# Optimization experiments

Measured on AMD Instinct MI355X. Metric: run time of the kernel, lower is better.

The kernel has to match this reference:

```python
import jax, jax.numpy as jnp
import numpy as np
import math

D_MODEL = 512
N_HEADS = 8
D_K = D_MODEL // N_HEADS
D_FF = 2048
EPS = 1e-6


def _layer_norm(x, gamma, beta):
    # Matches the torch module: unbiased std (ddof=1), divide by (std + eps)
    mean = jnp.mean(x, axis=-1, keepdims=True)
    std = jnp.std(x, axis=-1, ddof=1, keepdims=True)
    return gamma * (x - mean) / (std + EPS) + beta


def setup_inputs() -> dict:
    key = jax.random.key(0)
    ks = jax.random.split(key, 16)
    B, S = 4, 2048
    s_attn = 1.0 / math.sqrt(D_MODEL)
    s_ff1 = 1.0 / math.sqrt(D_MODEL)
    s_ff2 = 1.0 / math.sqrt(D_FF)
    inp = {
        "x": jax.random.normal(ks[0], (B, S, D_MODEL), dtype=jnp.float32),
        "mask": jnp.ones((1, 1, S, S), dtype=jnp.int32),
        "wq": jax.random.normal(ks[1], (D_MODEL, D_MODEL), jnp.float32) * s_attn,
        "bq": jnp.zeros((D_MODEL,), jnp.float32),
        "wk": jax.random.normal(ks[2], (D_MODEL, D_MODEL), jnp.float32) * s_attn,
        "bk": jnp.zeros((D_MODEL,), jnp.float32),
        "wv": jax.random.normal(ks[3], (D_MODEL, D_MODEL), jnp.float32) * s_attn,
        "bv": jnp.zeros((D_MODEL,), jnp.float32),
        "wo": jax.random.normal(ks[4], (D_MODEL, D_MODEL), jnp.float32) * s_attn,
        "bo": jnp.zeros((D_MODEL,), jnp.float32),
        "w1": jax.random.normal(ks[5], (D_MODEL, D_FF), jnp.float32) * s_ff1,
        "b1": jnp.zeros((D_FF,), jnp.float32),
        "w2": jax.random.normal(ks[6], (D_FF, D_MODEL), jnp.float32) * s_ff2,
        "b2": jnp.zeros((D_MODEL,), jnp.float32),
        "g1": jnp.ones((1, 1, D_MODEL), jnp.float32),
        "be1": jnp.zeros((1, 1, D_MODEL), jnp.float32),
        "g2": jnp.ones((1, 1, D_MODEL), jnp.float32),
        "be2": jnp.zeros((1, 1, D_MODEL), jnp.float32),
    }
    return inp


def reference(x, mask, wq, bq, wk, bk, wv, bv, wo, bo, w1, b1, w2, b2, g1, be1, g2, be2):
    B, S, _ = x.shape
    # --- residual 1: pre-norm self-attention ---
    xn = _layer_norm(x, g1, be1)
    q = (xn @ wq + bq).reshape(B, S, N_HEADS, D_K).transpose(0, 2, 1, 3)
    k = (xn @ wk + bk).reshape(B, S, N_HEADS, D_K).transpose(0, 2, 1, 3)
    v = (xn @ wv + bv).reshape(B, S, N_HEADS, D_K).transpose(0, 2, 1, 3)
    # NOTE: source uses floor division `//` by sqrt(d_k) (a faithful-ly kept bug)
    scores = jnp.floor_divide(jnp.einsum("bhqd,bhkd->bhqk", q, k), math.sqrt(D_K))
    scores = jnp.where(mask == 0, jnp.float32(-1e9), scores)
    attn = jax.nn.softmax(scores, axis=-1)
    ctx = jnp.einsum("bhqk,bhkd->bhqd", attn, v)
    ctx = ctx.transpose(0, 2, 1, 3).reshape(B, S, D_MODEL)
    x = x + (ctx @ wo + bo)
    # --- residual 2: pre-norm feed-forward ---
    xn2 = _layer_norm(x, g2, be2)
    ff = jax.nn.relu(xn2 @ w1 + b1) @ w2 + b2
    return x + ff
```

## Files before the change

kernel.cpp:

```cpp
#include <hip/hip_runtime.h>
#include <cmath>

#define SEQ 2048
#define DM 512
#define DFF 2048
#define NH 8
#define DKH 64
#define NROWS 8192

typedef __attribute__((ext_vector_type(8))) short bf16x8;
typedef __attribute__((ext_vector_type(16))) float f32x16;

__device__ __forceinline__ ushort f2bf(float f) {
    uint u = __float_as_uint(f);
    u += 0x7fff + ((u >> 16) & 1);
    return (ushort)(u >> 16);
}
__device__ __forceinline__ float bf2f(ushort h) {
    return __uint_as_float(((uint)h) << 16);
}
__device__ __forceinline__ uint cvtpk_bf16(float a, float b) {
    uint r;
    asm("v_cvt_pk_bf16_f32 %0, %1, %2" : "=v"(r) : "v"(a), "v"(b));
    return r;
}
__device__ __forceinline__ void gl_lds16(const void* g, void* l) {
    __builtin_amdgcn_global_load_lds(
        (const __attribute__((address_space(1))) void*)g,
        (__attribute__((address_space(3))) void*)l, 16, 0, 0);
}
__device__ __forceinline__ void* swz(char* base, int row, int col) {
    int byte = (row << 7) + (col << 1);
    byte ^= (row & 7) << 4;
    return base + byte;
}
__device__ __forceinline__ void* swzg(char* base, int row, int k) {
    int byte = (row << 7) + (k << 1);
    byte ^= ((row >> 2) & 7) << 4;
    return base + byte;
}

template<bool SPLIT>
__global__ __launch_bounds__(64) void ln_kernel(const float* __restrict__ x,
        const float* __restrict__ g, const float* __restrict__ b,
        ushort* __restrict__ oh, ushort* __restrict__ ol) {
    int row = blockIdx.x;
    int t = threadIdx.x;
    const float* xr = x + (size_t)row * DM + t * 8;
    float v[8];
    *(float4*)&v[0] = *(const float4*)(xr);
    *(float4*)&v[4] = *(const float4*)(xr + 4);
    float s = 0.f;
    #pragma unroll
    for (int j = 0; j < 8; ++j) s += v[j];
    #pragma unroll
    for (int m = 32; m > 0; m >>= 1) s += __shfl_xor(s, m);
    float mean = s * (1.0f / DM);
    float ss = 0.f;
    #pragma unroll
    for (int j = 0; j < 8; ++j) { float d = v[j] - mean; ss += d * d; }
    #pragma unroll
    for (int m = 32; m > 0; m >>= 1) ss += __shfl_xor(ss, m);
    float inv = 1.0f / (sqrtf(ss * (1.0f / (DM - 1))) + 1e-6f);
    float gv[8], bv[8];
    *(float4*)&gv[0] = *(const float4*)(g + t * 8);
    *(float4*)&gv[4] = *(const float4*)(g + t * 8 + 4);
    *(float4*)&bv[0] = *(const float4*)(b + t * 8);
    *(float4*)&bv[4] = *(const float4*)(b + t * 8 + 4);
    union { ushort us[8]; float4 f4; } ph, pl;
    #pragma unroll
    for (int j = 0; j < 8; ++j) {
        float o = gv[j] * (v[j] - mean) * inv + bv[j];
        ushort hb = f2bf(o);
        ph.us[j] = hb;
        if (SPLIT) pl.us[j] = f2bf(o - bf2f(hb));
    }
    *(float4*)(oh + (size_t)row * DM + t * 8) = ph.f4;
    if (SPLIT) *(float4*)(ol + (size_t)row * DM + t * 8) = pl.f4;
}

__global__ __launch_bounds__(256) void wconv4(
        const float* __restrict__ wq, const float* __restrict__ wk,
        const float* __restrict__ wv, const float* __restrict__ wo,
        ushort* __restrict__ qh, ushort* __restrict__ ql,
        ushort* __restrict__ kh, ushort* __restrict__ kl,
        ushort* __restrict__ vh, ushort* __restrict__ oh) {
    const int K = DM, N = DM;
    __shared__ float tile[64][65];
    int z = blockIdx.z;
    const float* W = (z == 0) ? wq : (z == 1) ? wk : (z == 2) ? wv : wo;
    ushort* Th = (z == 0) ? qh : (z == 1) ? kh : (z == 2) ? vh : oh;
    ushort* Tl = (z == 0) ? ql : (z == 1) ? kl : nullptr;
    bool split = (z < 2);
    int k0 = blockIdx.x * 64, n0 = blockIdx.y * 64;
    int t = threadIdx.x;
    {
        int kr = t >> 2, c0 = (t & 3) * 16;
        const float* src = W + (size_t)(k0 + kr) * N + n0 + c0;
        #pragma unroll
        for (int j = 0; j < 4; ++j)
            *(float4*)&tile[kr][c0 + j * 4] = *(const float4*)(src + j * 4);
    }
    __syncthreads();
    int n = t >> 2, kc = (t & 3) * 16;
    union { ushort us[16]; float4 f4[2]; } ph, pl;
    #pragma unroll
    for (int j = 0; j < 16; ++j) {
        float v = tile[kc + j][n];
        ushort hb = f2bf(v);
        ph.us[j] = hb;
        pl.us[j] = f2bf(v - bf2f(hb));
    }
    ushort* dh = Th + (size_t)(n0 + n) * K + k0 + kc;
    *(float4*)(dh) = ph.f4[0];
    *(float4*)(dh + 8) = ph.f4[1];
    if (split) {
        ushort* dl = Tl + (size_t)(n0 + n) * K + k0 + kc;
        *(float4*)(dl) = pl.f4[0];
        *(float4*)(dl + 8) = pl.f4[1];
    }
}

__global__ __launch_bounds__(256) void wconv(const float* __restrict__ W,
        ushort* __restrict__ Th, int K, int N) {
    __shared__ float tile[64][65];
    int k0 = blockIdx.x * 64, n0 = blockIdx.y * 64;
    int t = threadIdx.x;
    {
        int kr = t >> 2, c0 = (t & 3) * 16;
        const float* src = W + (size_t)(k0 + kr) * N + n0 + c0;
        #pragma unroll
        for (int j = 0; j < 4; ++j)
            *(float4*)&tile[kr][c0 + j * 4] = *(const float4*)(src + j * 4);
    }
    __syncthreads();
    int n = t >> 2, kc = (t & 3) * 16;
    union { ushort us[16]; float4 f4[2]; } ph;
    #pragma unroll
    for (int j = 0; j < 16; ++j) ph.us[j] = f2bf(tile[kc + j][n]);
    ushort* dh = Th + (size_t)(n0 + n) * K + k0 + kc;
    *(float4*)(dh) = ph.f4[0];
    *(float4*)(dh + 8) = ph.f4[1];
}

__global__ __launch_bounds__(256) void vtrans(const ushort* __restrict__ vh,
        ushort* __restrict__ vt) {
    __shared__ __align__(16) char tile[8192];
    int s0 = blockIdx.x * 64;
    int bh = blockIdx.y;
    int b = bh >> 3, h = bh & 7;
    int t = threadIdx.x;
    {
        int r = t >> 2, co = (t & 3) * 16;
        const ushort* src = vh + (size_t)(b * SEQ + s0 + r) * DM + h * DKH + co;
        *(float4*)swz(tile, r, co) = *(const float4*)(src);
        *(float4*)swz(tile, r, co + 8) = *(const float4*)(src + 8);
    }
    __syncthreads();
    int d = t >> 2, j0 = (t & 3) * 16;
    union { ushort us[16]; float4 f4[2]; } o;
    #pragma unroll
    for (int j = 0; j < 16; ++j)
        o.us[j] = *(ushort*)swz(tile, j0 + j, d);
    ushort* dst = vt + ((size_t)bh * DKH + d) * SEQ + s0 + j0;
    *(float4*)(dst) = o.f4[0];
    *(float4*)(dst + 8) = o.f4[1];
}

__global__ __launch_bounds__(256) void maskprep(const int* __restrict__ mask,
        ushort* __restrict__ mb) {
    int i = (blockIdx.x * 256 + threadIdx.x) * 8;
    int4 a = *(const int4*)(mask + i);
    int4 c = *(const int4*)(mask + i + 4);
    ushort neg = f2bf(-1e9f);
    union { ushort us[8]; float4 f4; } o;
    o.us[0] = a.x ? (ushort)0 : neg;
    o.us[1] = a.y ? (ushort)0 : neg;
    o.us[2] = a.z ? (ushort)0 : neg;
    o.us[3] = a.w ? (ushort)0 : neg;
    o.us[4] = c.x ? (ushort)0 : neg;
    o.us[5] = c.y ? (ushort)0 : neg;
    o.us[6] = c.z ? (ushort)0 : neg;
    o.us[7] = c.w ? (ushort)0 : neg;
    *(float4*)(mb + i) = o.f4;
}

template<bool RELU, bool HASRES, int OUT>
__global__ __launch_bounds__(256) void mgemm(
        const ushort* __restrict__ Ah, const ushort* __restrict__ Bth,
        const float* __restrict__ bias, const float* __restrict__ resid,
        float* __restrict__ Cf, ushort* __restrict__ Cbh,
        int M, int N, int K) {
    __shared__ __align__(16) char smem[65536];
    int tid = threadIdx.x;
    int lane = tid & 63, w = tid >> 6;
    int ln31 = lane & 31, hi = lane >> 5;
    int mh = (w >> 1) * 64, nh = (w & 1) * 64;
    int gx = gridDim.x;
    int nwg = gx * gridDim.y;
    int flat = blockIdx.y * gx + blockIdx.x;
    int sid = (flat & 7) * (nwg >> 3) + (flat >> 3);
    int n0 = (sid % gx) * 128;
    int m0 = (sid / gx) * 128;

    f32x16 acc[2][2];
    #pragma unroll
    for (int i = 0; i < 2; ++i)
        #pragma unroll
        for (int j = 0; j < 2; ++j)
            #pragma unroll
            for (int r = 0; r < 16; ++r) acc[i][j][r] = 0.f;

    auto stage = [&](char* Abuf, char* Bbuf, int k0) {
        #pragma unroll
        for (int c = 0; c < 4; ++c) {
            int ch = w * 4 + c;
            int r = ch * 8 + (lane >> 3);
            int u = (lane & 7) ^ ((r >> 2) & 7);
            gl_lds16(Ah + (size_t)(m0 + r) * K + k0 + u * 8, Abuf + ch * 1024);
            gl_lds16(Bth + (size_t)(n0 + r) * K + k0 + u * 8, Bbuf + ch * 1024);
        }
    };

    char* A0 = smem;
    char* B0 = smem + 16384;
    char* A1 = smem + 32768;
    char* B1 = smem + 49152;

    stage(A0, B0, 0);
    __syncthreads();
    int nk = K / 64;
    for (int kt = 0; kt < nk; ++kt) {
        char* Ac = (kt & 1) ? A1 : A0;
        char* Bc = (kt & 1) ? B1 : B0;
        if (kt + 1 < nk)
            stage((kt & 1) ? A0 : A1, (kt & 1) ? B0 : B1, (kt + 1) * 64);
        __builtin_amdgcn_s_setprio(1);
        #pragma unroll
        for (int km = 0; km < 4; ++km) {
            int kk = km * 16 + hi * 8;
            bf16x8 ah[2], bh[2];
            ah[0] = *(bf16x8*)swzg(Ac, mh + ln31, kk);
            ah[1] = *(bf16x8*)swzg(Ac, mh + 32 + ln31, kk);
            bh[0] = *(bf16x8*)swzg(Bc, nh + ln31, kk);
            bh[1] = *(bf16x8*)swzg(Bc, nh + 32 + ln31, kk);
            #pragma unroll
            for (int mi = 0; mi < 2; ++mi)
                #pragma unroll
                for (int ni = 0; ni < 2; ++ni)
                    acc[mi][ni] = __builtin_amdgcn_mfma_f32_32x32x16_bf16(
                        ah[mi], bh[ni], acc[mi][ni], 0, 0, 0);
        }
        __builtin_amdgcn_s_setprio(0);
        __syncthreads();
    }
    float bv[2];
    bv[0] = bias[n0 + nh + ln31];
    bv[1] = bias[n0 + nh + 32 + ln31];
    #pragma unroll
    for (int mi = 0; mi < 2; ++mi)
        #pragma unroll
        for (int ni = 0; ni < 2; ++ni) {
            int n = n0 + nh + ni * 32 + ln31;
            #pragma unroll
            for (int r = 0; r < 16; ++r) {
                int m = m0 + mh + mi * 32 + (r & 3) + 8 * (r >> 2) + 4 * hi;
                float v = acc[mi][ni][r] + bv[ni];
                if (HASRES) v += resid[(size_t)m * N + n];
                if (RELU) v = fmaxf(v, 0.f);
                size_t idx = (size_t)m * N + n;
                if (OUT == 0) Cf[idx] = v;
                else Cbh[idx] = f2bf(v);
            }
        }
}

__global__ __launch_bounds__(256) void qkv_gemm(
        const ushort* __restrict__ Ah, const ushort* __restrict__ Al,
        const ushort* __restrict__ Bth, const ushort* __restrict__ Btl,
        const float* __restrict__ bq, const float* __restrict__ bk,
        const float* __restrict__ bv_, ushort* __restrict__ q_h,
        ushort* __restrict__ q_l, ushort* __restrict__ k_h,
        ushort* __restrict__ k_l, ushort* __restrict__ v_h) {
    const int K = DM, N = DM;
    __shared__ __align__(16) char smem[65536];
    char* As_h = smem;
    char* Bs_h = smem + 16384;
    char* As_l = smem + 32768;
    char* Bs_l = smem + 49152;
    int tid = threadIdx.x;
    int lane = tid & 63, w = tid >> 6;
    int ln31 = lane & 31, hi = lane >> 5;
    int mh = (w >> 1) * 64, nh = (w & 1) * 64;
    int gx = gridDim.x;
    int nwg = gx * gridDim.y;
    int flat = blockIdx.y * gx + blockIdx.x;
    int sid = (flat & 7) * (nwg >> 3) + (flat >> 3);
    int n0 = (sid % gx) * 128;
    int m0 = (sid / gx) * 128;
    bool isqk = (n0 < 1024);

    f32x16 acc[2][2];
    #pragma unroll
    for (int i = 0; i < 2; ++i)
        #pragma unroll
        for (int j = 0; j < 2; ++j)
            #pragma unroll
            for (int r = 0; r < 16; ++r) acc[i][j][r] = 0.f;

    for (int k0 = 0; k0 < K; k0 += 64) {
        #pragma unroll
        for (int c = 0; c < 4; ++c) {
            int ch = w * 4 + c;
            int r = ch * 8 + (lane >> 3);
            int u = (lane & 7) ^ ((r >> 2) & 7);
            gl_lds16(Ah + (size_t)(m0 + r) * K + k0 + u * 8, As_h + ch * 1024);
            gl_lds16(Bth + (size_t)(n0 + r) * K + k0 + u * 8, Bs_h + ch * 1024);
            if (isqk) {
                gl_lds16(Al + (size_t)(m0 + r) * K + k0 + u * 8, As_l + ch * 1024);
                gl_lds16(Btl + (size_t)(n0 + r) * K + k0 + u * 8, Bs_l + ch * 1024);
            }
        }
        __syncthreads();
        __builtin_amdgcn_s_setprio(1);
        #pragma unroll
        for (int km = 0; km < 4; ++km) {
            int kk = km * 16 + hi * 8;
            bf16x8 ah[2], bh[2];
            ah[0] = *(bf16x8*)swzg(As_h, mh + ln31, kk);
            ah[1] = *(bf16x8*)swzg(As_h, mh + 32 + ln31, kk);
            bh[0] = *(bf16x8*)swzg(Bs_h, nh + ln31, kk);
            bh[1] = *(bf16x8*)swzg(Bs_h, nh + 32 + ln31, kk);
            if (isqk) {
                bf16x8 al[2], bl[2];
                al[0] = *(bf16x8*)swzg(As_l, mh + ln31, kk);
                al[1] = *(bf16x8*)swzg(As_l, mh + 32 + ln31, kk);
                bl[0] = *(bf16x8*)swzg(Bs_l, nh + ln31, kk);
                bl[1] = *(bf16x8*)swzg(Bs_l, nh + 32 + ln31, kk);
                #pragma unroll
                for (int mi = 0; mi < 2; ++mi)
                    #pragma unroll
                    for (int ni = 0; ni < 2; ++ni) {
                        acc[mi][ni] = __builtin_amdgcn_mfma_f32_32x32x16_bf16(
                            ah[mi], bh[ni], acc[mi][ni], 0, 0, 0);
                        acc[mi][ni] = __builtin_amdgcn_mfma_f32_32x32x16_bf16(
                            ah[mi], bl[ni], acc[mi][ni], 0, 0, 0);
                        acc[mi][ni] = __builtin_amdgcn_mfma_f32_32x32x16_bf16(
                            al[mi], bh[ni], acc[mi][ni], 0, 0, 0);
                    }
            } else {
                #pragma unroll
                for (int mi = 0; mi < 2; ++mi)
                    #pragma unroll
                    for (int ni = 0; ni < 2; ++ni)
                        acc[mi][ni] = __builtin_amdgcn_mfma_f32_32x32x16_bf16(
                            ah[mi], bh[ni], acc[mi][ni], 0, 0, 0);
            }
        }
        __builtin_amdgcn_s_setprio(0);
        __syncthreads();
    }
    const float* bias = (n0 < 512) ? bq : (n0 < 1024 ? bk : bv_);
    int ncol0 = n0 & 511;
    ushort* Oh = (n0 < 512) ? q_h : (n0 < 1024 ? k_h : v_h);
    ushort* Ol = (n0 < 512) ? q_l : (n0 < 1024 ? k_l : nullptr);
    float bvv[2];
    bvv[0] = bias[ncol0 + nh + ln31];
    bvv[1] = bias[ncol0 + nh + 32 + ln31];
    #pragma unroll
    for (int mi = 0; mi < 2; ++mi)
        #pragma unroll
        for (int ni = 0; ni < 2; ++ni) {
            int n = ncol0 + nh + ni * 32 + ln31;
            #pragma unroll
            for (int r = 0; r < 16; ++r) {
                int m = m0 + mh + mi * 32 + (r & 3) + 8 * (r >> 2) + 4 * hi;
                float v = acc[mi][ni][r] + bvv[ni];
                size_t idx = (size_t)m * N + n;
                ushort hb = f2bf(v);
                Oh[idx] = hb;
                if (isqk) Ol[idx] = f2bf(v - bf2f(hb));
            }
        }
}

__global__ __launch_bounds__(256, 3) void attn_kernel(
        const ushort* __restrict__ Qh, const ushort* __restrict__ Ql,
        const ushort* __restrict__ Khg, const ushort* __restrict__ Klg,
        const ushort* __restrict__ Vtg, const ushort* __restrict__ mb,
        ushort* __restrict__ O) {
    __shared__ __align__(16) char smem[49152];
    int tid = threadIdx.x;
    int w = tid >> 6, lane = tid & 63;
    int ln31 = lane & 31, hi = lane >> 5;
    bool hib = (hi != 0);
    int f = blockIdx.y * gridDim.x + blockIdx.x;
    int g = (f & 7) * 64 + (f >> 3);
    int qb = g & 15, bh = g >> 4;
    int b = bh >> 3, h = bh & 7;
    int q0 = qb * 128;
    size_t brow = (size_t)b * SEQ;
    int hcol = h * DKH;

    auto stage_kv = [&](char* buf, int kt) {
        #pragma unroll
        for (int c = 0; c < 2; ++c) {
            int ch = w * 2 + c;
            int r = ch * 8 + (lane >> 3);
            int u = (lane & 7) ^ (r & 7);
            gl_lds16(Khg + (brow + kt * 64 + r) * DM + hcol + u * 8,
                     buf + ch * 1024);
            gl_lds16(Klg + (brow + kt * 64 + r) * DM + hcol + u * 8,
                     buf + 8192 + ch * 1024);
            gl_lds16(Vtg + ((size_t)bh * DKH + r) * SEQ + kt * 64 + u * 8,
                     buf + 16384 + ch * 1024);
        }
    };

    {
        char* QhL = smem;
        char* QlL = smem + 16384;
        #pragma unroll
        for (int c = 0; c < 4; ++c) {
            int ch = w * 4 + c;
            int r = ch * 8 + (lane >> 3);
            int u = (lane & 7) ^ (r & 7);
            gl_lds16(Qh + (brow + q0 + r) * DM + hcol + u * 8, QhL + ch * 1024);
            gl_lds16(Ql + (brow + q0 + r) * DM + hcol + u * 8, QlL + ch * 1024);
        }
    }
    __syncthreads();
    bf16x8 qfh[4], qfl[4];
    {
        int qr = w * 32 + ln31;
        #pragma unroll
        for (int c = 0; c < 4; ++c) {
            qfh[c] = *(bf16x8*)swz(smem, qr, c * 16 + hi * 8);
            qfl[c] = *(bf16x8*)swz(smem + 16384, qr, c * 16 + hi * 8);
        }
    }
    __syncthreads();
    stage_kv(smem, 0);
    __syncthreads();

    f32x16 ctx0, ctx1;
    #pragma unroll
    for (int r = 0; r < 16; ++r) { ctx0[r] = 0.f; ctx1[r] = 0.f; }
    float m_i = -1e30f, l_i = 0.f;
    int qglob = q0 + w * 32 + ln31;
    const ushort* mrow = mb + (size_t)qglob * SEQ;

    for (int kt = 0; kt < SEQ / 64; ++kt) {
        char* cur = smem + (kt & 1) * 24576;
        if (kt + 1 < SEQ / 64)
            stage_kv(smem + ((kt + 1) & 1) * 24576, kt + 1);
        ushort4 mpre[8];
        #pragma unroll
        for (int i = 0; i < 8; ++i)
            mpre[i] = *(const ushort4*)(mrow + kt * 64 + i * 8 + hi * 4);
        char* KhL = cur;
        char* KlL = cur + 8192;
        char* VtL = cur + 16384;
        #pragma unroll
        for (int ksub = 0; ksub < 2; ++ksub) {
            f32x16 s;
            #pragma unroll
            for (int r = 0; r < 16; ++r) s[r] = 0.f;
            __builtin_amdgcn_s_setprio(1);
            #pragma unroll
            for (int c = 0; c < 4; ++c) {
                bf16x8 ka = *(bf16x8*)swz(KhL, ksub * 32 + ln31, c * 16 + hi * 8);
                bf16x8 kb = *(bf16x8*)swz(KlL, ksub * 32 + ln31, c * 16 + hi * 8);
                s = __builtin_amdgcn_mfma_f32_32x32x16_bf16(ka, qfh[c], s, 0, 0, 0);
                s = __builtin_amdgcn_mfma_f32_32x32x16_bf16(ka, qfl[c], s, 0, 0, 0);
                s = __builtin_amdgcn_mfma_f32_32x32x16_bf16(kb, qfh[c], s, 0, 0, 0);
            }
            __builtin_amdgcn_s_setprio(0);
            float tmax = -1e30f;
            #pragma unroll
            for (int rg = 0; rg < 4; ++rg) {
                ushort4 mv = mpre[ksub * 4 + rg];
                ushort mu[4] = {mv.x, mv.y, mv.z, mv.w};
                #pragma unroll
                for (int j = 0; j < 4; ++j) {
                    int r = rg * 4 + j;
                    float sc = floorf(s[r] * 0.125f) + bf2f(mu[j]);
                    s[r] = sc;
                    tmax = fmaxf(tmax, sc);
                }
            }
            tmax = fmaxf(tmax, __shfl_xor(tmax, 32));
            if (!__all(tmax <= m_i)) {
                float newm = fmaxf(m_i, tmax);
                float scl = __expf(m_i - newm);
                m_i = newm;
                l_i *= scl;
                #pragma unroll
                for (int r = 0; r < 16; ++r) { ctx0[r] *= scl; ctx1[r] *= scl; }
            }
            float psum = 0.f;
            #pragma unroll
            for (int r = 0; r < 16; ++r) {
                float p = __expf(s[r] - m_i);
                s[r] = p;
                psum += p;
            }
            psum += __shfl_xor(psum, 32);
            l_i += psum;
            uint pk0[4], pk1[4];
            #pragma unroll
            for (int rg = 0; rg < 4; ++rg) {
                pk0[rg] = cvtpk_bf16(s[rg * 4 + 0], s[rg * 4 + 1]);
                pk1[rg] = cvtpk_bf16(s[rg * 4 + 2], s[rg * 4 + 3]);
            }
            __builtin_amdgcn_s_setprio(1);
            #pragma unroll
            for (int cc = 0; cc < 2; ++cc) {
                uint A0 = pk0[cc * 2], A1 = pk1[cc * 2];
                uint B0 = pk0[cc * 2 + 1], B1 = pk1[cc * 2 + 1];
                uint send0 = hib ? A0 : B0;
                uint send1 = hib ? A1 : B1;
                uint own0  = hib ? B0 : A0;
                uint own1  = hib ? B1 : A1;
                uint recv0 = (uint)__shfl_xor((int)send0, 32);
                uint recv1 = (uint)__shfl_xor((int)send1, 32);
                union { uint u[4]; bf16x8 v; } pb;
                pb.u[0] = hib ? recv0 : own0;
                pb.u[1] = hib ? recv1 : own1;
                pb.u[2] = hib ? own0 : recv0;
                pb.u[3] = hib ? own1 : recv1;
                int c = ksub * 2 + cc;
                bf16x8 va0 = *(bf16x8*)swz(VtL, ln31, c * 16 + hi * 8);
                bf16x8 va1 = *(bf16x8*)swz(VtL, 32 + ln31, c * 16 + hi * 8);
                ctx0 = __builtin_amdgcn_mfma_f32_32x32x16_bf16(va0, pb.v, ctx0, 0, 0, 0);
                ctx1 = __builtin_amdgcn_mfma_f32_32x32x16_bf16(va1, pb.v, ctx1, 0, 0, 0);
            }
            __builtin_amdgcn_s_setprio(0);
        }
        __syncthreads();
    }

    float inv = 1.0f / l_i;
    ushort* op = O + (brow + qglob) * DM + hcol;
    #pragma unroll
    for (int r = 0; r < 16; ++r) {
        int d = (r & 3) + 8 * (r >> 2) + 4 * hi;
        op[d] = f2bf(ctx0[r] * inv);
        op[32 + d] = f2bf(ctx1[r] * inv);
    }
}

extern "C" void kernel_launch(void* const* d_in, const int* in_sizes, int n_in,
                              void* d_out, int out_size, void* d_ws, size_t ws_size,
                              hipStream_t stream) {
    const float* x    = (const float*)d_in[0];
    const int*   mask = (const int*)d_in[1];
    const float* wq = (const float*)d_in[2];
    const float* bq = (const float*)d_in[3];
    const float* wk = (const float*)d_in[4];
    const float* bk = (const float*)d_in[5];
    const float* wv = (const float*)d_in[6];
    const float* bv = (const float*)d_in[7];
    const float* wo = (const float*)d_in[8];
    const float* bo = (const float*)d_in[9];
    const float* w1 = (const float*)d_in[10];
    const float* b1 = (const float*)d_in[11];
    const float* w2 = (const float*)d_in[12];
    const float* b2 = (const float*)d_in[13];
    const float* g1  = (const float*)d_in[14];
    const float* be1 = (const float*)d_in[15];
    const float* g2  = (const float*)d_in[16];
    const float* be2 = (const float*)d_in[17];
    float* out = (float*)d_out;

    char* ws = (char*)d_ws;
    const size_t MiB = 1024 * 1024;
    ushort* xn_h = (ushort*)(ws);
    ushort* xn_l = (ushort*)(ws + 8 * MiB);
    ushort* q_h  = (ushort*)(ws + 16 * MiB);
    ushort* q_l  = (ushort*)(ws + 24 * MiB);
    ushort* k_h  = (ushort*)(ws + 32 * MiB);
    ushort* k_l  = (ushort*)(ws + 40 * MiB);
    ushort* v_h  = (ushort*)(ws + 48 * MiB);
    ushort* v_t  = (ushort*)(ws + 56 * MiB);
    ushort* wqkvt_h = (ushort*)(ws + 64 * MiB);
    ushort* wqkvt_l = (ushort*)(ws + 66 * MiB);
    ushort* wot_h = (ushort*)(ws + 67 * MiB);
    ushort* w1t_h = (ushort*)(ws + 68 * MiB);
    ushort* w2t_h = (ushort*)(ws + 70 * MiB);
    ushort* mb    = (ushort*)(ws + 72 * MiB);
    ushort* ctx  = xn_h;
    ushort* xn2  = xn_l;
    ushort* ff1  = q_h;

    dim3 blk256(256);
    wconv4<<<dim3(8, 8, 4), blk256, 0, stream>>>(
        wq, wk, wv, wo, wqkvt_h, wqkvt_l, wqkvt_h + 512 * 512,
        wqkvt_l + 512 * 512, wqkvt_h + 1024 * 512, wot_h);
    wconv<<<dim3(8, 32), blk256, 0, stream>>>(w1, w1t_h, DM, DFF);
    wconv<<<dim3(32, 8), blk256, 0, stream>>>(w2, w2t_h, DFF, DM);
    maskprep<<<SEQ * SEQ / 8 / 256, blk256, 0, stream>>>(mask, mb);
    ln_kernel<true><<<NROWS, 64, 0, stream>>>(x, g1, be1, xn_h, xn_l);
    qkv_gemm<<<dim3(12, NROWS / 128), blk256, 0, stream>>>(
        xn_h, xn_l, wqkvt_h, wqkvt_l, bq, bk, bv, q_h, q_l, k_h, k_l, v_h);
    vtrans<<<dim3(SEQ / 64, 4 * NH), blk256, 0, stream>>>(v_h, v_t);
    {
        dim3 grid(SEQ / 128, 4 * NH);
        attn_kernel<<<grid, blk256, 0, stream>>>(q_h, q_l, k_h, k_l, v_t, mb, ctx);
    }
    {
        dim3 grid(DM / 128, NROWS / 128);
        mgemm<false,true,0><<<grid, blk256, 0, stream>>>(
            ctx, wot_h, bo, x, out, nullptr, NROWS, DM, DM);
    }
    ln_kernel<false><<<NROWS, 64, 0, stream>>>(out, g2, be2, xn2, nullptr);
    {
        dim3 grid(DFF / 128, NROWS / 128);
        mgemm<true,false,1><<<grid, blk256, 0, stream>>>(
            xn2, w1t_h, b1, nullptr, nullptr, ff1, NROWS, DFF, DM);
    }
    {
        dim3 grid(DM / 128, NROWS / 128);
        mgemm<false,true,0><<<grid, blk256, 0, stream>>>(
            ff1, w2t_h, b2, out, out, nullptr, NROWS, DM, DFF);
    }
}
```

Baseline: 240.7 us.

## Split attention over key halves with combine kernel and skip all-ones mask tiles

The attention kernel now splits the key range into two halves, doubling the grid to 1024 blocks. Each block writes unnormalized partial context plus its running max and sum, and a new combine kernel merges the two halves flash-decoding style. maskprep also builds per-row, per-64-key-tile flags marking tiles where the mask is all ones, so the attention loop skips the mask loads and adds there. This raises occupancy and cuts mask memory traffic, at the cost of an extra kernel, partial-result round trips through global memory, and bf16 rounding of the unnormalized partials.

```diff
diff --git a/kernel.cpp b/kernel.cpp
--- a/kernel.cpp
+++ b/kernel.cpp
@@ -167,22 +167,39 @@
     *(float4*)(dst + 8) = o.f4[1];
 }
 
-__global__ __launch_bounds__(256) void maskprep(const int* __restrict__ mask,
-        ushort* __restrict__ mb) {
-    int i = (blockIdx.x * 256 + threadIdx.x) * 8;
-    int4 a = *(const int4*)(mask + i);
-    int4 c = *(const int4*)(mask + i + 4);
+__global__ __launch_bounds__(64) void maskprep(const int* __restrict__ mask,
+        ushort* __restrict__ mb, unsigned char* __restrict__ mflag) {
+    int row = blockIdx.x;
+    int lane = threadIdx.x;
     ushort neg = f2bf(-1e9f);
-    union { ushort us[8]; float4 f4; } o;
-    o.us[0] = a.x ? (ushort)0 : neg;
-    o.us[1] = a.y ? (ushort)0 : neg;
-    o.us[2] = a.z ? (ushort)0 : neg;
-    o.us[3] = a.w ? (ushort)0 : neg;
-    o.us[4] = c.x ? (ushort)0 : neg;
-    o.us[5] = c.y ? (ushort)0 : neg;
-    o.us[6] = c.z ? (ushort)0 : neg;
-    o.us[7] = c.w ? (ushort)0 : neg;
-    *(float4*)(mb + i) = o.f4;
+    unsigned long long bal[4];
+    #pragma unroll
+    for (int u = 0; u < 4; ++u) {
+        int base = row * SEQ + u * 512 + lane * 8;
+        int4 a = *(const int4*)(mask + base);
+        int4 c = *(const int4*)(mask + base + 4);
+        union { ushort us[8]; float4 f4; } o;
+        o.us[0] = a.x ? (ushort)0 : neg;
+        o.us[1] = a.y ? (ushort)0 : neg;
+        o.us[2] = a.z ? (ushort)0 : neg;
+        o.us[3] = a.w ? (ushort)0 : neg;
+        o.us[4] = c.x ? (ushort)0 : neg;
+        o.us[5] = c.y ? (ushort)0 : neg;
+        o.us[6] = c.z ? (ushort)0 : neg;
+        o.us[7] = c.w ? (ushort)0 : neg;
+        *(float4*)(mb + base) = o.f4;
+        bool ok = a.x && a.y && a.z && a.w && c.x && c.y && c.z && c.w;
+        bal[u] = __ballot(ok);
+    }
+    if (lane < 32) {
+        int u = lane >> 3;
+        unsigned long long bsel = bal[0];
+        bsel = (u == 1) ? bal[1] : bsel;
+        bsel = (u == 2) ? bal[2] : bsel;
+        bsel = (u == 3) ? bal[3] : bsel;
+        int byte = (int)((bsel >> ((lane & 7) * 8)) & 0xFFull);
+        mflag[row * 32 + lane] = (byte == 0xFF) ? 1 : 0;
+    }
 }
 
 template<bool RELU, bool HASRES, int OUT>
@@ -388,19 +405,23 @@
         const ushort* __restrict__ Qh, const ushort* __restrict__ Ql,
         const ushort* __restrict__ Khg, const ushort* __restrict__ Klg,
         const ushort* __restrict__ Vtg, const ushort* __restrict__ mb,
-        ushort* __restrict__ O) {
+        const unsigned char* __restrict__ mflag,
+        ushort* __restrict__ pctx0, ushort* __restrict__ pctx1,
+        float2* __restrict__ ml) {
     __shared__ __align__(16) char smem[49152];
     int tid = threadIdx.x;
     int w = tid >> 6, lane = tid & 63;
     int ln31 = lane & 31, hi = lane >> 5;
     bool hib = (hi != 0);
     int f = blockIdx.y * gridDim.x + blockIdx.x;
-    int g = (f & 7) * 64 + (f >> 3);
-    int qb = g & 15, bh = g >> 4;
+    int g = (f & 7) * 128 + (f >> 3);
+    int bh = g >> 5, rest = g & 31;
+    int part = rest >> 4, qb = rest & 15;
     int b = bh >> 3, h = bh & 7;
     int q0 = qb * 128;
     size_t brow = (size_t)b * SEQ;
     int hcol = h * DKH;
+    int ktbeg = part * 16, ktend = ktbeg + 16;
 
     auto stage_kv = [&](char* buf, int kt) {
         #pragma unroll
@@ -440,7 +461,7 @@
         }
     }
     __syncthreads();
-    stage_kv(smem, 0);
+    stage_kv(smem + (ktbeg & 1) * 24576, ktbeg);
     __syncthreads();
 
     f32x16 ctx0, ctx1;
@@ -450,14 +471,18 @@
     int qglob = q0 + w * 32 + ln31;
     const ushort* mrow = mb + (size_t)qglob * SEQ;
 
-    for (int kt = 0; kt < SEQ / 64; ++kt) {
+    for (int kt = ktbeg; kt < ktend; ++kt) {
         char* cur = smem + (kt & 1) * 24576;
-        if (kt + 1 < SEQ / 64)
+        if (kt + 1 < ktend)
             stage_kv(smem + ((kt + 1) & 1) * 24576, kt + 1);
+        unsigned char fl = mflag[qglob * 32 + kt];
+        bool domask = !__all(fl != 0);
         ushort4 mpre[8];
-        #pragma unroll
-        for (int i = 0; i < 8; ++i)
-            mpre[i] = *(const ushort4*)(mrow + kt * 64 + i * 8 + hi * 4);
+        if (domask) {
+            #pragma unroll
+            for (int i = 0; i < 8; ++i)
+                mpre[i] = *(const ushort4*)(mrow + kt * 64 + i * 8 + hi * 4);
+        }
         char* KhL = cur;
         char* KlL = cur + 8192;
         char* VtL = cur + 16384;
@@ -477,14 +502,23 @@
             }
             __builtin_amdgcn_s_setprio(0);
             float tmax = -1e30f;
-            #pragma unroll
-            for (int rg = 0; rg < 4; ++rg) {
-                ushort4 mv = mpre[ksub * 4 + rg];
-                ushort mu[4] = {mv.x, mv.y, mv.z, mv.w};
+            if (domask) {
                 #pragma unroll
-                for (int j = 0; j < 4; ++j) {
-                    int r = rg * 4 + j;
-                    float sc = floorf(s[r] * 0.125f) + bf2f(mu[j]);
+                for (int rg = 0; rg < 4; ++rg) {
+                    ushort4 mv = mpre[ksub * 4 + rg];
+                    ushort mu[4] = {mv.x, mv.y, mv.z, mv.w};
+                    #pragma unroll
+                    for (int j = 0; j < 4; ++j) {
+                        int r = rg * 4 + j;
+                        float sc = floorf(s[r] * 0.125f) + bf2f(mu[j]);
+                        s[r] = sc;
+                        tmax = fmaxf(tmax, sc);
+                    }
+                }
+            } else {
+                #pragma unroll
+                for (int r = 0; r < 16; ++r) {
+                    float sc = floorf(s[r] * 0.125f);
                     s[r] = sc;
                     tmax = fmaxf(tmax, sc);
                 }
@@ -540,14 +574,42 @@
         __syncthreads();
     }
 
-    float inv = 1.0f / l_i;
-    ushort* op = O + (brow + qglob) * DM + hcol;
+    ushort* P = part ? pctx1 : pctx0;
+    size_t pbase = ((size_t)bh * SEQ + qglob) * DKH;
     #pragma unroll
     for (int r = 0; r < 16; ++r) {
         int d = (r & 3) + 8 * (r >> 2) + 4 * hi;
-        op[d] = f2bf(ctx0[r] * inv);
-        op[32 + d] = f2bf(ctx1[r] * inv);
-    }
+        P[pbase + d] = f2bf(ctx0[r]);
+        P[pbase + 32 + d] = f2bf(ctx1[r]);
+    }
+    if (hi == 0)
+        ml[((size_t)part * 32 + bh) * SEQ + qglob] = make_float2(m_i, l_i);
+}
+
+__global__ __launch_bounds__(256) void attn_combine(
+        const ushort* __restrict__ p0, const ushort* __restrict__ p1,
+        const float2* __restrict__ ml, ushort* __restrict__ O) {
+    int idx = blockIdx.x * 256 + threadIdx.x;
+    int d0 = (idx & 7) * 8;
+    int q = (idx >> 3) & (SEQ - 1);
+    int bh = idx >> 14;
+    int b = bh >> 3, h = bh & 7;
+    size_t pb = ((size_t)bh * SEQ + q) * DKH + d0;
+    bf16x8 c0 = *(const bf16x8*)(p0 + pb);
+    bf16x8 c1 = *(const bf16x8*)(p1 + pb);
+    float2 e0 = ml[(size_t)bh * SEQ + q];
+    float2 e1 = ml[((size_t)32 + bh) * SEQ + q];
+    float m = fmaxf(e0.x, e1.x);
+    float w0 = __expf(e0.x - m), w1 = __expf(e1.x - m);
+    float inv = 1.0f / (e0.y * w0 + e1.y * w1);
+    union { ushort us[8]; float4 f4; } o;
+    #pragma unroll
+    for (int j = 0; j < 8; ++j) {
+        float v0 = bf2f((ushort)c0[j]);
+        float v1 = bf2f((ushort)c1[j]);
+        o.us[j] = f2bf((v0 * w0 + v1 * w1) * inv);
+    }
+    *(float4*)(O + ((size_t)(b * SEQ + q)) * DM + h * DKH + d0) = o.f4;
 }
 
 extern "C" void kernel_launch(void* const* d_in, const int* in_sizes, int n_in,
@@ -586,9 +648,13 @@
     ushort* wqkvt_h = (ushort*)(ws + 64 * MiB);
     ushort* wqkvt_l = (ushort*)(ws + 66 * MiB);
     ushort* wot_h = (ushort*)(ws + 67 * MiB);
+    unsigned char* mflag = (unsigned char*)(ws + 67 * MiB + 512 * 1024);
     ushort* w1t_h = (ushort*)(ws + 68 * MiB);
     ushort* w2t_h = (ushort*)(ws + 70 * MiB);
     ushort* mb    = (ushort*)(ws + 72 * MiB);
+    ushort* pctx0 = (ushort*)(ws + 80 * MiB);
+    ushort* pctx1 = (ushort*)(ws + 88 * MiB);
+    float2* ml    = (float2*)(ws + 64 * MiB);
     ushort* ctx  = xn_h;
     ushort* xn2  = xn_l;
     ushort* ff1  = q_h;
@@ -599,15 +665,17 @@
         wqkvt_l + 512 * 512, wqkvt_h + 1024 * 512, wot_h);
     wconv<<<dim3(8, 32), blk256, 0, stream>>>(w1, w1t_h, DM, DFF);
     wconv<<<dim3(32, 8), blk256, 0, stream>>>(w2, w2t_h, DFF, DM);
-    maskprep<<<SEQ * SEQ / 8 / 256, blk256, 0, stream>>>(mask, mb);
+    maskprep<<<SEQ, 64, 0, stream>>>(mask, mb, mflag);
     ln_kernel<true><<<NROWS, 64, 0, stream>>>(x, g1, be1, xn_h, xn_l);
     qkv_gemm<<<dim3(12, NROWS / 128), blk256, 0, stream>>>(
         xn_h, xn_l, wqkvt_h, wqkvt_l, bq, bk, bv, q_h, q_l, k_h, k_l, v_h);
     vtrans<<<dim3(SEQ / 64, 4 * NH), blk256, 0, stream>>>(v_h, v_t);
     {
-        dim3 grid(SEQ / 128, 4 * NH);
-        attn_kernel<<<grid, blk256, 0, stream>>>(q_h, q_l, k_h, k_l, v_t, mb, ctx);
-    }
+        dim3 grid(32, 32);
+        attn_kernel<<<grid, blk256, 0, stream>>>(
+            q_h, q_l, k_h, k_l, v_t, mb, mflag, pctx0, pctx1, ml);
+    }
+    attn_combine<<<32 * SEQ * 8 / 256, blk256, 0, stream>>>(pctx0, pctx1, ml, ctx);
     {
         dim3 grid(DM / 128, NROWS / 128);
         mgemm<false,true,0><<<grid, blk256, 0, stream>>>(
```

Measured after the change: 238.2 us. No clear change (-1.1%).
